# Kernel tuning notes

Hardware: AMD Instinct MI355X
Metric: run time of the kernel (lower is better)

The kernel has to match this reference:

```python
import jax, jax.numpy as jnp
import numpy as np

TREE = 128
BASIC = 128
EPS = 1e-5


def layer_norm(x, g, b):
    m = jnp.mean(x, axis=-1, keepdims=True)
    v = jnp.mean((x - m) ** 2, axis=-1, keepdims=True)
    return (x - m) * jax.lax.rsqrt(v + EPS) * g + b


def setup_inputs() -> dict:
    key = jax.random.key(0)
    ks = jax.random.split(key, 32)
    n2, n1, n0 = 320000, 80000, 20000
    inp = {
        'subtree_h_top': jax.random.normal(ks[0], (n2, TREE), jnp.float32),
        'atom_x_1': jax.random.normal(ks[1], (n1, BASIC), jnp.float32),
        'atom_x_0': jax.random.normal(ks[2], (n0, BASIC), jnp.float32),
        'bond_x_2': jax.random.normal(ks[3], (n2, BASIC), jnp.float32),
        'bond_x_1': jax.random.normal(ks[4], (n1, BASIC), jnp.float32),
        'branch_W1': jax.random.normal(ks[5], (2, TREE + BASIC, TREE), jnp.float32) * 0.05,
        'branch_b1': jnp.zeros((2, TREE), jnp.float32),
        'branch_g1': jnp.ones((2, TREE), jnp.float32),
        'branch_beta1': jnp.zeros((2, TREE), jnp.float32),
        'branch_W2': jax.random.normal(ks[6], (2, TREE, TREE), jnp.float32) * 0.05,
        'branch_b2': jnp.zeros((2, TREE), jnp.float32),
        'branch_g2': jnp.ones((2, TREE), jnp.float32),
        'branch_beta2': jnp.zeros((2, TREE), jnp.float32),
        'sub_W1': jax.random.normal(ks[7], (2, BASIC + TREE, TREE), jnp.float32) * 0.05,
        'sub_b1': jnp.zeros((2, TREE), jnp.float32),
        'sub_g1': jnp.ones((2, TREE), jnp.float32),
        'sub_beta1': jnp.zeros((2, TREE), jnp.float32),
        'sub_W2': jax.random.normal(ks[8], (2, TREE, TREE), jnp.float32) * 0.05,
        'sub_b2': jnp.zeros((2, TREE), jnp.float32),
        'sub_g2': jnp.ones((2, TREE), jnp.float32),
        'sub_beta2': jnp.zeros((2, TREE), jnp.float32),
        'head_W': jax.random.normal(ks[9], (2, BASIC + TREE, TREE), jnp.float32) * 0.05,
        'head_b': jnp.zeros((2, TREE), jnp.float32),
        'head_g': jnp.ones((2, TREE), jnp.float32),
        'head_beta': jnp.zeros((2, TREE), jnp.float32),
        'src_2': jax.random.randint(ks[10], (n2,), 0, n2),
        'dst_2': jax.random.randint(ks[11], (n2,), 0, n1),
        'src_1': jax.random.randint(ks[12], (n1,), 0, n1),
        'dst_1': jax.random.randint(ks[13], (n1,), 0, n0),
    }
    return inp


def reference(subtree_h_top, atom_x_1, atom_x_0, bond_x_2, bond_x_1,
              branch_W1, branch_b1, branch_g1, branch_beta1,
              branch_W2, branch_b2, branch_g2, branch_beta2,
              sub_W1, sub_b1, sub_g1, sub_beta1,
              sub_W2, sub_b2, sub_g2, sub_beta2,
              head_W, head_b, head_g, head_beta,
              src_2, dst_2, src_1, dst_1):
    relu = jax.nn.relu
    h = subtree_h_top  # subtree_h of level tree_level nodes
    atom_xs = (atom_x_1, atom_x_0)
    bond_xs = (bond_x_2, bond_x_1)
    srcs = (src_2, src_1)
    dsts = (dst_2, dst_1)
    for i in range(2):  # i=0 -> k=2, i=1 -> k=1 (fixed small loop over tree levels)
        ax = atom_xs[i]
        # Branch_Update: edge MLP on [subtree_h[src], bond_x]
        ex = jnp.concatenate([h[srcs[i]], bond_xs[i]], axis=-1)  # [E, tree+basic]
        bh = relu(layer_norm(ex @ branch_W1[i] + branch_b1[i], branch_g1[i], branch_beta1[i]))
        bh = relu(layer_norm(bh @ branch_W2[i] + branch_b2[i], branch_g2[i], branch_beta2[i]))
        # fn.sum aggregation per destination (head) node
        agg = jax.ops.segment_sum(bh, dsts[i], num_segments=ax.shape[0])
        # Tree_Update_Sep
        sx = jnp.concatenate([ax, agg], axis=-1)  # [N, basic+tree]
        f = relu(layer_norm(sx @ sub_W1[i] + sub_b1[i], sub_g1[i], sub_beta1[i]))
        f = relu(layer_norm(f @ sub_W2[i] + sub_b2[i], sub_g2[i], sub_beta2[i]))
        th = jnp.concatenate([ax, f], axis=-1)
        h = relu(layer_norm(th @ head_W[i] + head_b[i], head_g[i], head_beta[i]))
    return h  # subtree_h of atom_0 nodes: [n0, tree_dim]
```

## Files before the change

### kernel.cpp

```cpp
#include <hip/hip_runtime.h>


#define D   128
#define TE  64
#define XS  264

typedef float  f32x4 __attribute__((ext_vector_type(4)));
typedef _Float16 f16x8 __attribute__((ext_vector_type(8)));

__device__ __forceinline__ unsigned short f2h(float f) {
    union { _Float16 h; unsigned short u; } x;
    x.h = (_Float16)f;
    return x.u;
}

__global__ __launch_bounds__(256) void pack_w(
    const float* __restrict__ brW1, const float* __restrict__ brW2,
    const float* __restrict__ sW1,  const float* __restrict__ sW2,
    const float* __restrict__ hW,   unsigned short* __restrict__ Wp)
{
    int p = blockIdx.x * 256 + threadIdx.x;
    const float* src; int off, K;
    if (p < 65536)       { src = brW1; off = 0;      K = 256; }
    else if (p < 98304)  { src = brW2; off = 65536;  K = 128; }
    else if (p < 163840) { src = sW1;  off = 98304;  K = 256; }
    else if (p < 196608) { src = sW2;  off = 163840; K = 128; }
    else                 { src = hW;   off = 196608; K = 256; }
    int q = p - off, lvl, r;
    if (K == 256) { lvl = q >> 15; r = q & 32767; }
    else          { lvl = q >> 14; r = q & 16383; }
    int kb = r >> 12, n = (r >> 5) & 127, kk = r & 31;
    Wp[p] = f2h(src[(size_t)lvl * K * 128 + (size_t)(kb * 32 + kk) * 128 + n]);
}


__global__ __launch_bounds__(256) void csr_hist(
    const int* __restrict__ dA, int EA, const int* __restrict__ dB, int EB,
    int* __restrict__ cnt, int AOFFv)
{
    int i = blockIdx.x * 256 + threadIdx.x;
    if (i < EA)               atomicAdd(cnt + dA[i], 1);
    else if (i - EA < EB)     atomicAdd(cnt + AOFFv + dB[i - EA], 1);
}

__global__ __launch_bounds__(256) void csr_scanA(
    const int* __restrict__ cnt, int* __restrict__ inc, int* __restrict__ bsum,
    int nbA, int AOFFv)
{
    __shared__ int lds[256];
    int b = blockIdx.x, t = threadIdx.x;
    int lb, ebase, bs;
    if (b < nbA) { lb = b;       ebase = 0;     bs = lb; }
    else         { lb = b - nbA; ebase = AOFFv; bs = 128 + lb; }
    int idx = ebase + lb * 1024 + t * 4;
    int s0 = cnt[idx], s1 = cnt[idx + 1], s2 = cnt[idx + 2], s3 = cnt[idx + 3];
    int p1 = s0 + s1, p2 = p1 + s2, p3 = p2 + s3;
    lds[t] = p3; __syncthreads();
#pragma unroll
    for (int o = 1; o < 256; o <<= 1) {
        int v = (t >= o) ? lds[t - o] : 0;
        __syncthreads();
        lds[t] += v;
        __syncthreads();
    }
    int ex = lds[t] - p3;
    inc[idx] = ex + s0; inc[idx + 1] = ex + p1; inc[idx + 2] = ex + p2; inc[idx + 3] = ex + p3;
    if (t == 255) bsum[bs] = lds[255];
}

__global__ __launch_bounds__(256) void csr_scanB(int* __restrict__ bsum, int nbA, int nbB)
{
    __shared__ int lds[256];
    int t = threadIdx.x, seg = t >> 7, i = t & 127;
    int n = seg ? nbB : nbA;
    lds[t] = (i < n) ? bsum[t] : 0;
    __syncthreads();
#pragma unroll
    for (int o = 1; o < 128; o <<= 1) {
        int v = (i >= o) ? lds[t - o] : 0;
        __syncthreads();
        lds[t] += v;
        __syncthreads();
    }
    if (i < n) bsum[t] = lds[t];
}

__global__ __launch_bounds__(256) void csr_scanC(
    const int* __restrict__ cnt, int* __restrict__ inc, const int* __restrict__ bsum,
    int* __restrict__ cursor, int nbA, int AOFFv)
{
    int b = blockIdx.x, t = threadIdx.x;
    int lb, ebase, bs;
    if (b < nbA) { lb = b;       ebase = 0;     bs = lb; }
    else         { lb = b - nbA; ebase = AOFFv; bs = 128 + lb; }
    int carry = (lb > 0) ? bsum[bs - 1] : 0;
    int idx = ebase + lb * 1024 + t * 4;
#pragma unroll
    for (int j = 0; j < 4; ++j) {
        int v = inc[idx + j] + carry;
        inc[idx + j] = v;
        cursor[idx + j] = v - cnt[idx + j];
    }
}

__global__ __launch_bounds__(256) void csr_pos(
    const int* __restrict__ dA, int EA, const int* __restrict__ dB, int EB,
    int* __restrict__ cursor, int* __restrict__ posA, int* __restrict__ posB, int AOFFv)
{
    int i = blockIdx.x * 256 + threadIdx.x;
    if (i < EA)           posA[i] = atomicAdd(cursor + dA[i], 1);
    else if (i - EA < EB) posB[i - EA] = atomicAdd(cursor + AOFFv + dB[i - EA], 1);
}


template<int KB>
__device__ __forceinline__ void gemm_f16(const unsigned short* s_in, int stride,
    const unsigned short* __restrict__ Wp, int rb, int cb, int n15, int q, f32x4 acc[2][4])
{
    f32x4 zero = {0.f, 0.f, 0.f, 0.f};
#pragma unroll
    for (int m = 0; m < 2; ++m)
#pragma unroll
        for (int ct = 0; ct < 4; ++ct) acc[m][ct] = zero;
#pragma unroll
    for (int kb = 0; kb < KB; ++kb) {
        f16x8 af0 = *(const f16x8*)(s_in + (rb + n15) * stride + kb * 32 + q * 8);
        f16x8 af1 = *(const f16x8*)(s_in + (rb + 16 + n15) * stride + kb * 32 + q * 8);
        const unsigned short* wb = Wp + (size_t)kb * 4096 + q * 8;
#pragma unroll
        for (int ct = 0; ct < 4; ++ct) {
            f16x8 bf = *(const f16x8*)(wb + (cb + ct * 16 + n15) * 32);
            acc[0][ct] = __builtin_amdgcn_mfma_f32_16x16x32_f16(af0, bf, acc[0][ct], 0, 0, 0);
            acc[1][ct] = __builtin_amdgcn_mfma_f32_16x16x32_f16(af1, bf, acc[1][ct], 0, 0, 0);
        }
    }
}

__device__ __forceinline__ void ln_relu(f32x4 acc[2][4],
    const float* __restrict__ b, const float* __restrict__ g, const float* __restrict__ be,
    float* s_red, float* s_ms, int rb, int cb, int n15, int q, int wcol, int t)
{
#pragma unroll
    for (int ct = 0; ct < 4; ++ct) {
        float bb = b[cb + ct * 16 + n15];
#pragma unroll
        for (int m = 0; m < 2; ++m)
#pragma unroll
            for (int r = 0; r < 4; ++r) acc[m][ct][r] += bb;
    }
    float sum[2][4], ss[2][4];
#pragma unroll
    for (int m = 0; m < 2; ++m)
#pragma unroll
        for (int r = 0; r < 4; ++r) {
            sum[m][r] = acc[m][0][r] + acc[m][1][r] + acc[m][2][r] + acc[m][3][r];
            ss[m][r]  = acc[m][0][r]*acc[m][0][r] + acc[m][1][r]*acc[m][1][r]
                      + acc[m][2][r]*acc[m][2][r] + acc[m][3][r]*acc[m][3][r];
        }
#pragma unroll
    for (int off = 1; off < 16; off <<= 1) {
#pragma unroll
        for (int m = 0; m < 2; ++m)
#pragma unroll
            for (int r = 0; r < 4; ++r) {
                sum[m][r] += __shfl_xor(sum[m][r], off, 64);
                ss[m][r]  += __shfl_xor(ss[m][r],  off, 64);
            }
    }
    if (n15 == 0) {
#pragma unroll
        for (int m = 0; m < 2; ++m)
#pragma unroll
            for (int r = 0; r < 4; ++r) {
                int row = rb + m * 16 + q * 4 + r;
                s_red[row * 4 + wcol * 2 + 0] = sum[m][r];
                s_red[row * 4 + wcol * 2 + 1] = ss[m][r];
            }
    }
    __syncthreads();
    if (t < TE) {
        float sm = s_red[t * 4 + 0] + s_red[t * 4 + 2];
        float sq = s_red[t * 4 + 1] + s_red[t * 4 + 3];
        float mean = sm * (1.f / 128.f);
        float var  = sq * (1.f / 128.f) - mean * mean;
        s_ms[t * 2 + 0] = mean;
        s_ms[t * 2 + 1] = rsqrtf(var + 1e-5f);
    }
    __syncthreads();
#pragma unroll
    for (int ct = 0; ct < 4; ++ct) {
        float gg = g[cb + ct * 16 + n15], bb = be[cb + ct * 16 + n15];
#pragma unroll
        for (int m = 0; m < 2; ++m)
#pragma unroll
            for (int r = 0; r < 4; ++r) {
                int row = rb + m * 16 + q * 4 + r;
                float v = (acc[m][ct][r] - s_ms[row * 2 + 0]) * s_ms[row * 2 + 1] * gg + bb;
                acc[m][ct][r] = fmaxf(v, 0.f);
            }
    }
}

template<bool HBF16, bool CSR>
__global__ __launch_bounds__(256, 4) void edge_mlp(
    const void* __restrict__ hsrc, const float* __restrict__ bond,
    const int* __restrict__ src, const int* __restrict__ dstpos,
    const unsigned short* __restrict__ Wp1, const unsigned short* __restrict__ Wp2,
    const float* __restrict__ b1, const float* __restrict__ g1, const float* __restrict__ be1,
    const float* __restrict__ b2, const float* __restrict__ g2, const float* __restrict__ be2,
    float* __restrict__ agg, unsigned short* __restrict__ ebh, int E)
{
    __shared__ unsigned short s_x[TE * XS];
    __shared__ float s_red[TE * 4];
    __shared__ float s_ms[TE * 2];
    __shared__ int s_src[TE], s_idx[TE];
    unsigned short* s_y = s_x + 128;

    int t = threadIdx.x, eb = blockIdx.x * TE;
    if (t < TE) {
        int ge = eb + t;
        s_src[t] = (ge < E) ? src[ge] : -1;
        s_idx[t] = (ge < E) ? dstpos[ge] : -1;
    }
    __syncthreads();

    if (HBF16) {
        const unsigned short* hp = (const unsigned short*)hsrc;
        for (int c = t; c < TE * 16; c += 256) {
            int row = c >> 4, k8 = c & 15;
            int s = s_src[row];
            uint4 v = make_uint4(0, 0, 0, 0);
            if (s >= 0) v = *(const uint4*)(hp + (size_t)s * 128 + k8 * 8);
            *(uint4*)(s_x + row * XS + k8 * 8) = v;
        }
    } else {
        const float* hp = (const float*)hsrc;
        for (int c = t; c < TE * 32; c += 256) {
            int row = c >> 5, k4 = c & 31;
            int s = s_src[row];
            float4 v = make_float4(0, 0, 0, 0);
            if (s >= 0) v = *(const float4*)(hp + (size_t)s * 128 + k4 * 4);
            ushort4 o; o.x = f2h(v.x); o.y = f2h(v.y); o.z = f2h(v.z); o.w = f2h(v.w);
            *(ushort4*)(s_x + row * XS + k4 * 4) = o;
        }
    }
    for (int c = t; c < TE * 32; c += 256) {
        int row = c >> 5, k4 = c & 31;
        int ge = eb + row;
        float4 v = make_float4(0, 0, 0, 0);
        if (ge < E) v = *(const float4*)(bond + (size_t)ge * 128 + k4 * 4);
        ushort4 o; o.x = f2h(v.x); o.y = f2h(v.y); o.z = f2h(v.z); o.w = f2h(v.w);
        *(ushort4*)(s_x + row * XS + 128 + k4 * 4) = o;
    }
    __syncthreads();

    int l = t & 63, w = t >> 6;
    int n15 = l & 15, q = l >> 4;
    int rb = (w & 1) * 32, cb = (w >> 1) * 64, wcol = w >> 1;

    f32x4 acc[2][4];
    gemm_f16<8>(s_x, XS, Wp1, rb, cb, n15, q, acc);
    ln_relu(acc, b1, g1, be1, s_red, s_ms, rb, cb, n15, q, wcol, t);
#pragma unroll
    for (int m = 0; m < 2; ++m)
#pragma unroll
        for (int ct = 0; ct < 4; ++ct)
#pragma unroll
            for (int r = 0; r < 4; ++r)
                s_y[(rb + m * 16 + q * 4 + r) * XS + cb + ct * 16 + n15] = f2h(acc[m][ct][r]);
    __syncthreads();
    gemm_f16<4>(s_y, XS, Wp2, rb, cb, n15, q, acc);
    ln_relu(acc, b2, g2, be2, s_red, s_ms, rb, cb, n15, q, wcol, t);

    if (CSR) {
#pragma unroll
        for (int m = 0; m < 2; ++m)
#pragma unroll
            for (int ct = 0; ct < 4; ++ct)
#pragma unroll
                for (int r = 0; r < 4; ++r)
                    s_x[(rb + m * 16 + q * 4 + r) * XS + cb + ct * 16 + n15] = f2h(acc[m][ct][r]);
        __syncthreads();
        for (int c = t; c < TE * 16; c += 256) {
            int row = c >> 4, k8 = c & 15;
            int p = s_idx[row];
            if (p >= 0)
                *(uint4*)(ebh + (size_t)p * 128 + k8 * 8) =
                    *(const uint4*)(s_x + row * XS + k8 * 8);
        }
    } else {
#pragma unroll
        for (int m = 0; m < 2; ++m)
#pragma unroll
            for (int ct = 0; ct < 4; ++ct)
#pragma unroll
                for (int r = 0; r < 4; ++r) {
                    int row = rb + m * 16 + q * 4 + r;
                    int gd = s_idx[row];
                    if (gd >= 0)
                        atomicAdd(agg + (size_t)gd * D + cb + ct * 16 + n15, acc[m][ct][r]);
                }
    }
}

template<bool OUT_F16, bool CSR>
__global__ __launch_bounds__(256, 4) void node_mlp(
    const float* __restrict__ ax, const float* __restrict__ agg,
    const int* __restrict__ inc, const unsigned short* __restrict__ ebh,
    const unsigned short* __restrict__ Wp1, const unsigned short* __restrict__ Wp2,
    const unsigned short* __restrict__ Wp3,
    const float* __restrict__ b1, const float* __restrict__ g1, const float* __restrict__ be1,
    const float* __restrict__ b2, const float* __restrict__ g2, const float* __restrict__ be2,
    const float* __restrict__ b3, const float* __restrict__ g3, const float* __restrict__ be3,
    void* __restrict__ out, int N)
{
    __shared__ unsigned short s_x[TE * XS];
    __shared__ float s_red[TE * 4];
    __shared__ float s_ms[TE * 2];
    __shared__ int s_beg[TE], s_end[TE];
    unsigned short* s_y = s_x + 128;

    int t = threadIdx.x, nb = blockIdx.x * TE;

    if (CSR && t < TE) {
        int gr = nb + t, b0 = 0, e0 = 0;
        if (gr < N) { e0 = inc[gr]; b0 = (gr == 0) ? 0 : inc[gr - 1]; }
        s_beg[t] = b0; s_end[t] = e0;
    }

    for (int c = t; c < TE * 32; c += 256) {
        int row = c >> 5, k4 = c & 31;
        int gr = nb + row;
        float4 v = make_float4(0, 0, 0, 0);
        if (gr < N) v = *(const float4*)(ax + (size_t)gr * 128 + k4 * 4);
        ushort4 o; o.x = f2h(v.x); o.y = f2h(v.y); o.z = f2h(v.z); o.w = f2h(v.w);
        *(ushort4*)(s_x + row * XS + k4 * 4) = o;
    }

    if (CSR) {
        __syncthreads();
        int r = t >> 2, s4 = t & 3;
        float a[32];
#pragma unroll
        for (int k = 0; k < 32; ++k) a[k] = 0.f;
        int jb = s_beg[r], je = s_end[r];
        for (int j = jb; j < je; ++j) {
            const unsigned short* rp = ebh + (size_t)j * 128 + s4 * 32;
            f16x8 v0 = *(const f16x8*)rp;
            f16x8 v1 = *(const f16x8*)(rp + 8);
            f16x8 v2 = *(const f16x8*)(rp + 16);
            f16x8 v3 = *(const f16x8*)(rp + 24);
#pragma unroll
            for (int k = 0; k < 8; ++k) {
                a[k]      += (float)v0[k];
                a[8 + k]  += (float)v1[k];
                a[16 + k] += (float)v2[k];
                a[24 + k] += (float)v3[k];
            }
        }
        unsigned short* op = s_x + r * XS + 128 + s4 * 32;
#pragma unroll
        for (int blk = 0; blk < 4; ++blk) {
            f16x8 h;
#pragma unroll
            for (int k = 0; k < 8; ++k) h[k] = (_Float16)a[blk * 8 + k];
            *(f16x8*)(op + blk * 8) = h;
        }
    } else {
        for (int c = t; c < TE * 32; c += 256) {
            int row = c >> 5, k4 = c & 31;
            int gr = nb + row;
            float4 v = make_float4(0, 0, 0, 0);
            if (gr < N) v = *(const float4*)(agg + (size_t)gr * 128 + k4 * 4);
            ushort4 o; o.x = f2h(v.x); o.y = f2h(v.y); o.z = f2h(v.z); o.w = f2h(v.w);
            *(ushort4*)(s_x + row * XS + 128 + k4 * 4) = o;
        }
    }
    __syncthreads();

    int l = t & 63, w = t >> 6;
    int n15 = l & 15, q = l >> 4;
    int rb = (w & 1) * 32, cb = (w >> 1) * 64, wcol = w >> 1;

    f32x4 acc[2][4];
    gemm_f16<8>(s_x, XS, Wp1, rb, cb, n15, q, acc);
    ln_relu(acc, b1, g1, be1, s_red, s_ms, rb, cb, n15, q, wcol, t);
#pragma unroll
    for (int m = 0; m < 2; ++m)
#pragma unroll
        for (int ct = 0; ct < 4; ++ct)
#pragma unroll
            for (int r = 0; r < 4; ++r)
                s_y[(rb + m * 16 + q * 4 + r) * XS + cb + ct * 16 + n15] = f2h(acc[m][ct][r]);
    __syncthreads();
    gemm_f16<4>(s_y, XS, Wp2, rb, cb, n15, q, acc);
    ln_relu(acc, b2, g2, be2, s_red, s_ms, rb, cb, n15, q, wcol, t);
#pragma unroll
    for (int m = 0; m < 2; ++m)
#pragma unroll
        for (int ct = 0; ct < 4; ++ct)
#pragma unroll
            for (int r = 0; r < 4; ++r)
                s_x[(rb + m * 16 + q * 4 + r) * XS + 128 + cb + ct * 16 + n15] = f2h(acc[m][ct][r]);
    __syncthreads();
    gemm_f16<8>(s_x, XS, Wp3, rb, cb, n15, q, acc);
    ln_relu(acc, b3, g3, be3, s_red, s_ms, rb, cb, n15, q, wcol, t);

#pragma unroll
    for (int m = 0; m < 2; ++m)
#pragma unroll
        for (int ct = 0; ct < 4; ++ct)
#pragma unroll
            for (int r = 0; r < 4; ++r) {
                int row = rb + m * 16 + q * 4 + r;
                int gr = nb + row;
                int col = cb + ct * 16 + n15;
                if (gr < N) {
                    if (OUT_F16)
                        ((unsigned short*)out)[(size_t)gr * D + col] = f2h(acc[m][ct][r]);
                    else
                        ((float*)out)[(size_t)gr * D + col] = acc[m][ct][r];
                }
            }
}

extern "C" void kernel_launch(void* const* d_in, const int* in_sizes, int n_in,
                              void* d_out, int out_size, void* d_ws, size_t ws_size,
                              hipStream_t stream)
{
    const float* h2   = (const float*)d_in[0];
    const float* ax1  = (const float*)d_in[1];
    const float* ax0  = (const float*)d_in[2];
    const float* bx2  = (const float*)d_in[3];
    const float* bx1  = (const float*)d_in[4];
    const float* brW1 = (const float*)d_in[5];
    const float* brb1 = (const float*)d_in[6];
    const float* brg1 = (const float*)d_in[7];
    const float* brbe1= (const float*)d_in[8];
    const float* brW2 = (const float*)d_in[9];
    const float* brb2 = (const float*)d_in[10];
    const float* brg2 = (const float*)d_in[11];
    const float* brbe2= (const float*)d_in[12];
    const float* sW1  = (const float*)d_in[13];
    const float* sb1  = (const float*)d_in[14];
    const float* sg1  = (const float*)d_in[15];
    const float* sbe1 = (const float*)d_in[16];
    const float* sW2  = (const float*)d_in[17];
    const float* sb2  = (const float*)d_in[18];
    const float* sg2  = (const float*)d_in[19];
    const float* sbe2 = (const float*)d_in[20];
    const float* hW   = (const float*)d_in[21];
    const float* hb   = (const float*)d_in[22];
    const float* hg   = (const float*)d_in[23];
    const float* hbe  = (const float*)d_in[24];
    const int*   src2 = (const int*)d_in[25];
    const int*   dst2 = (const int*)d_in[26];
    const int*   src1 = (const int*)d_in[27];
    const int*   dst1 = (const int*)d_in[28];

    int n2 = in_sizes[0] / D;
    int n1 = in_sizes[1] / D;
    int n0 = in_sizes[2] / D;

    unsigned short* Wp = (unsigned short*)d_ws;

    const unsigned short* pBr1[2] = { Wp + 0,      Wp + 32768 };
    const unsigned short* pBr2[2] = { Wp + 65536,  Wp + 65536  + 16384 };
    const unsigned short* pS1 [2] = { Wp + 98304,  Wp + 98304  + 32768 };
    const unsigned short* pS2 [2] = { Wp + 163840, Wp + 163840 + 16384 };
    const unsigned short* pH  [2] = { Wp + 196608, Wp + 196608 + 32768 };

    int nbA = (n1 + 1023) / 1024, nbB = (n0 + 1023) / 1024;
    int AOFFv = nbA * 1024;
    size_t AN = (size_t)AOFFv + (size_t)nbB * 1024;
    auto al = [](size_t x) { return (x + 255) & ~(size_t)255; };
    size_t o = 524288;
    size_t cnt_o  = o; o = al(o + AN * 4);
    size_t inc_o  = o; o = al(o + AN * 4);
    size_t cur_o  = o; o = al(o + AN * 4);
    size_t bsum_o = o; o = al(o + 1024);
    size_t posA_o = o; o = al(o + (size_t)n2 * 4);
    size_t posB_o = o; o = al(o + (size_t)n1 * 4);
    size_t h1_o   = o; o = al(o + (size_t)n1 * 256);
    size_t ebh_o  = o; o = al(o + (size_t)n2 * 256);
    bool use_csr = (ws_size >= o) && (nbA <= 128) && (nbB <= 128);

    pack_w<<<dim3(1024), dim3(256), 0, stream>>>(brW1, brW2, sW1, sW2, hW, Wp);

    if (use_csr) {
        int*            cnt    = (int*)((char*)d_ws + cnt_o);
        int*            inc    = (int*)((char*)d_ws + inc_o);
        int*            cursor = (int*)((char*)d_ws + cur_o);
        int*            bsum   = (int*)((char*)d_ws + bsum_o);
        int*            posA   = (int*)((char*)d_ws + posA_o);
        int*            posB   = (int*)((char*)d_ws + posB_o);
        unsigned short* h1     = (unsigned short*)((char*)d_ws + h1_o);
        unsigned short* ebh    = (unsigned short*)((char*)d_ws + ebh_o);

        int EG = (n2 + n1 + 255) / 256;
        hipMemsetAsync(cnt, 0, AN * 4, stream);
        csr_hist <<<dim3(EG),        dim3(256), 0, stream>>>(dst2, n2, dst1, n1, cnt, AOFFv);
        csr_scanA<<<dim3(nbA + nbB), dim3(256), 0, stream>>>(cnt, inc, bsum, nbA, AOFFv);
        csr_scanB<<<dim3(1),         dim3(256), 0, stream>>>(bsum, nbA, nbB);
        csr_scanC<<<dim3(nbA + nbB), dim3(256), 0, stream>>>(cnt, inc, bsum, cursor, nbA, AOFFv);
        csr_pos  <<<dim3(EG),        dim3(256), 0, stream>>>(dst2, n2, dst1, n1, cursor, posA, posB, AOFFv);

        edge_mlp<false, true><<<dim3((n2 + TE - 1) / TE), dim3(256), 0, stream>>>(
            h2, bx2, src2, posA, pBr1[0], pBr2[0],
            brb1, brg1, brbe1, brb2, brg2, brbe2, nullptr, ebh, n2);
        node_mlp<true, true><<<dim3((n1 + TE - 1) / TE), dim3(256), 0, stream>>>(
            ax1, nullptr, inc, ebh, pS1[0], pS2[0], pH[0],
            sb1, sg1, sbe1, sb2, sg2, sbe2, hb, hg, hbe, h1, n1);

        edge_mlp<true, true><<<dim3((n1 + TE - 1) / TE), dim3(256), 0, stream>>>(
            h1, bx1, src1, posB, pBr1[1], pBr2[1],
            brb1 + D, brg1 + D, brbe1 + D, brb2 + D, brg2 + D, brbe2 + D, nullptr, ebh, n1);
        node_mlp<false, true><<<dim3((n0 + TE - 1) / TE), dim3(256), 0, stream>>>(
            ax0, nullptr, inc + AOFFv, ebh, pS1[1], pS2[1], pH[1],
            sb1 + D, sg1 + D, sbe1 + D, sb2 + D, sg2 + D, sbe2 + D,
            hb + D, hg + D, hbe + D, d_out, n0);
    } else {
        float*          agg = (float*)((char*)d_ws + 524288);
        unsigned short* h1  = (unsigned short*)(agg + (size_t)n1 * D);

        hipMemsetAsync(agg, 0, (size_t)n1 * D * sizeof(float), stream);
        edge_mlp<false, false><<<dim3((n2 + TE - 1) / TE), dim3(256), 0, stream>>>(
            h2, bx2, src2, dst2, pBr1[0], pBr2[0],
            brb1, brg1, brbe1, brb2, brg2, brbe2, agg, nullptr, n2);
        node_mlp<true, false><<<dim3((n1 + TE - 1) / TE), dim3(256), 0, stream>>>(
            ax1, agg, nullptr, nullptr, pS1[0], pS2[0], pH[0],
            sb1, sg1, sbe1, sb2, sg2, sbe2, hb, hg, hbe, h1, n1);

        hipMemsetAsync(agg, 0, (size_t)n0 * D * sizeof(float), stream);
        edge_mlp<true, false><<<dim3((n1 + TE - 1) / TE), dim3(256), 0, stream>>>(
            h1, bx1, src1, dst1, pBr1[1], pBr2[1],
            brb1 + D, brg1 + D, brbe1 + D, brb2 + D, brg2 + D, brbe2 + D, agg, nullptr, n1);
        node_mlp<false, false><<<dim3((n0 + TE - 1) / TE), dim3(256), 0, stream>>>(
            ax0, agg, nullptr, nullptr, pS1[1], pS2[1], pH[1],
            sb1 + D, sg1 + D, sbe1 + D, sb2 + D, sg2 + D, sbe2 + D,
            hb + D, hg + D, hbe + D, d_out, n0);
    }
}
```

Before: 682.6 us.

## Add persistent prefetching edge MLP and pre-convert subtree features to fp16

Adds a persistent-block edge MLP kernel that loads the next tile's gathered h rows, bond rows and destination positions into registers while the current tile's two GEMM+LayerNorm stages run. This hides gather latency behind compute. A separate conversion kernel first turns the top-level subtree_h into fp16, so the random gather reads half the bytes. node_mlp becomes grid-strided with a capped grid. The new path needs extra workspace, and the kernel drops occupancy to 3 blocks per SM because of the added prefetch registers.

```diff
diff --git a/kernel.cpp b/kernel.cpp
--- a/kernel.cpp
+++ b/kernel.cpp
@@ -33,6 +33,22 @@
     Wp[p] = f2h(src[(size_t)lvl * K * 128 + (size_t)(kb * 32 + kk) * 128 + n]);
 }
 
+__global__ __launch_bounds__(256) void conv_h(
+    const float* __restrict__ in, unsigned short* __restrict__ out, long n)
+{
+    long i = (long)blockIdx.x * 256 + threadIdx.x;
+    long stride = (long)gridDim.x * 256;
+    for (; i < n; i += stride) {
+        float4 a = ((const float4*)in)[i * 2];
+        float4 b = ((const float4*)in)[i * 2 + 1];
+        ushort4 o1, o2;
+        o1.x = f2h(a.x); o1.y = f2h(a.y); o1.z = f2h(a.z); o1.w = f2h(a.w);
+        o2.x = f2h(b.x); o2.y = f2h(b.y); o2.z = f2h(b.z); o2.w = f2h(b.w);
+        ((ushort4*)out)[i * 2]     = o1;
+        ((ushort4*)out)[i * 2 + 1] = o2;
+    }
+}
+
 
 __global__ __launch_bounds__(256) void csr_hist(
     const int* __restrict__ dA, int EA, const int* __restrict__ dB, int EB,
@@ -201,6 +217,124 @@
     }
 }
 
+__global__ __launch_bounds__(256, 3) void edge_mlp_pf(
+    const unsigned short* __restrict__ hsrc, const float* __restrict__ bond,
+    const int* __restrict__ src, const int* __restrict__ dstpos,
+    const unsigned short* __restrict__ Wp1, const unsigned short* __restrict__ Wp2,
+    const float* __restrict__ b1, const float* __restrict__ g1, const float* __restrict__ be1,
+    const float* __restrict__ b2, const float* __restrict__ g2, const float* __restrict__ be2,
+    unsigned short* __restrict__ ebh, int E, int ntiles)
+{
+    __shared__ unsigned short s_x[TE * XS];
+    __shared__ float s_red[TE * 4];
+    __shared__ float s_ms[TE * 2];
+    unsigned short* s_y = s_x + 128;
+
+    int t = threadIdx.x;
+    int l = t & 63, w = t >> 6;
+    int n15 = l & 15, q = l >> 4;
+    int rb = (w & 1) * 32, cb = (w >> 1) * 64, wcol = w >> 1;
+    int hrow = t >> 4, k8 = t & 15;
+    int brow = t >> 5, k4 = t & 31;
+
+    int tile0 = blockIdx.x;
+    if (tile0 >= ntiles) return;
+
+    int cidx[4];
+    {
+        int eb = tile0 * TE;
+#pragma unroll
+        for (int j = 0; j < 4; ++j) {
+            int ge = eb + hrow + 16 * j;
+            int sv = (ge < E) ? src[ge] : -1;
+            cidx[j] = (ge < E) ? dstpos[ge] : -1;
+            uint4 v = make_uint4(0, 0, 0, 0);
+            if (sv >= 0) v = *(const uint4*)(hsrc + (size_t)sv * 128 + k8 * 8);
+            *(uint4*)(s_x + (hrow + 16 * j) * XS + k8 * 8) = v;
+        }
+#pragma unroll
+        for (int i = 0; i < 8; ++i) {
+            int ge = eb + brow + 8 * i;
+            float4 v = make_float4(0, 0, 0, 0);
+            if (ge < E) v = *(const float4*)(bond + (size_t)ge * 128 + k4 * 4);
+            ushort4 o; o.x = f2h(v.x); o.y = f2h(v.y); o.z = f2h(v.z); o.w = f2h(v.w);
+            *(ushort4*)(s_x + (brow + 8 * i) * XS + 128 + k4 * 4) = o;
+        }
+    }
+
+    for (int tile = tile0; tile < ntiles; tile += gridDim.x) {
+        __syncthreads();
+
+        int ntile = tile + gridDim.x;
+        bool has_next = (ntile < ntiles);
+        uint4  ph[4];
+        float4 pb[8];
+        int    nidx[4];
+        if (has_next) {
+            int eb = ntile * TE;
+#pragma unroll
+            for (int j = 0; j < 4; ++j) {
+                int ge = eb + hrow + 16 * j;
+                int sv = (ge < E) ? src[ge] : -1;
+                nidx[j] = (ge < E) ? dstpos[ge] : -1;
+                ph[j] = make_uint4(0, 0, 0, 0);
+                if (sv >= 0) ph[j] = *(const uint4*)(hsrc + (size_t)sv * 128 + k8 * 8);
+            }
+#pragma unroll
+            for (int i = 0; i < 8; ++i) {
+                int ge = eb + brow + 8 * i;
+                pb[i] = make_float4(0, 0, 0, 0);
+                if (ge < E) pb[i] = *(const float4*)(bond + (size_t)ge * 128 + k4 * 4);
+            }
+            __builtin_amdgcn_sched_barrier(0);
+        }
+
+        f32x4 acc[2][4];
+        gemm_f16<8>(s_x, XS, Wp1, rb, cb, n15, q, acc);
+        ln_relu(acc, b1, g1, be1, s_red, s_ms, rb, cb, n15, q, wcol, t);
+#pragma unroll
+        for (int m = 0; m < 2; ++m)
+#pragma unroll
+            for (int ct = 0; ct < 4; ++ct)
+#pragma unroll
+                for (int r = 0; r < 4; ++r)
+                    s_y[(rb + m * 16 + q * 4 + r) * XS + cb + ct * 16 + n15] = f2h(acc[m][ct][r]);
+        __syncthreads();
+        gemm_f16<4>(s_y, XS, Wp2, rb, cb, n15, q, acc);
+        ln_relu(acc, b2, g2, be2, s_red, s_ms, rb, cb, n15, q, wcol, t);
+
+#pragma unroll
+        for (int m = 0; m < 2; ++m)
+#pragma unroll
+            for (int ct = 0; ct < 4; ++ct)
+#pragma unroll
+                for (int r = 0; r < 4; ++r)
+                    s_x[(rb + m * 16 + q * 4 + r) * XS + cb + ct * 16 + n15] = f2h(acc[m][ct][r]);
+        __syncthreads();
+#pragma unroll
+        for (int j = 0; j < 4; ++j) {
+            if (cidx[j] >= 0)
+                *(uint4*)(ebh + (size_t)cidx[j] * 128 + k8 * 8) =
+                    *(const uint4*)(s_x + (hrow + 16 * j) * XS + k8 * 8);
+        }
+        __syncthreads();
+
+        if (has_next) {
+#pragma unroll
+            for (int j = 0; j < 4; ++j)
+                *(uint4*)(s_x + (hrow + 16 * j) * XS + k8 * 8) = ph[j];
+#pragma unroll
+            for (int i = 0; i < 8; ++i) {
+                ushort4 o;
+                o.x = f2h(pb[i].x); o.y = f2h(pb[i].y); o.z = f2h(pb[i].z); o.w = f2h(pb[i].w);
+                *(ushort4*)(s_x + (brow + 8 * i) * XS + 128 + k4 * 4) = o;
+            }
+#pragma unroll
+            for (int j = 0; j < 4; ++j) cidx[j] = nidx[j];
+        }
+    }
+}
+
 template<bool HBF16, bool CSR>
 __global__ __launch_bounds__(256, 4) void edge_mlp(
     const void* __restrict__ hsrc, const float* __restrict__ bond,
@@ -312,7 +446,7 @@
     const float* __restrict__ b1, const float* __restrict__ g1, const float* __restrict__ be1,
     const float* __restrict__ b2, const float* __restrict__ g2, const float* __restrict__ be2,
     const float* __restrict__ b3, const float* __restrict__ g3, const float* __restrict__ be3,
-    void* __restrict__ out, int N)
+    void* __restrict__ out, int N, int ntiles)
 {
     __shared__ unsigned short s_x[TE * XS];
     __shared__ float s_red[TE * 4];
@@ -320,108 +454,110 @@
     __shared__ int s_beg[TE], s_end[TE];
     unsigned short* s_y = s_x + 128;
 
-    int t = threadIdx.x, nb = blockIdx.x * TE;
-
-    if (CSR && t < TE) {
-        int gr = nb + t, b0 = 0, e0 = 0;
-        if (gr < N) { e0 = inc[gr]; b0 = (gr == 0) ? 0 : inc[gr - 1]; }
-        s_beg[t] = b0; s_end[t] = e0;
-    }
-
-    for (int c = t; c < TE * 32; c += 256) {
-        int row = c >> 5, k4 = c & 31;
-        int gr = nb + row;
-        float4 v = make_float4(0, 0, 0, 0);
-        if (gr < N) v = *(const float4*)(ax + (size_t)gr * 128 + k4 * 4);
-        ushort4 o; o.x = f2h(v.x); o.y = f2h(v.y); o.z = f2h(v.z); o.w = f2h(v.w);
-        *(ushort4*)(s_x + row * XS + k4 * 4) = o;
-    }
-
-    if (CSR) {
-        __syncthreads();
-        int r = t >> 2, s4 = t & 3;
-        float a[32];
-#pragma unroll
-        for (int k = 0; k < 32; ++k) a[k] = 0.f;
-        int jb = s_beg[r], je = s_end[r];
-        for (int j = jb; j < je; ++j) {
-            const unsigned short* rp = ebh + (size_t)j * 128 + s4 * 32;
-            f16x8 v0 = *(const f16x8*)rp;
-            f16x8 v1 = *(const f16x8*)(rp + 8);
-            f16x8 v2 = *(const f16x8*)(rp + 16);
-            f16x8 v3 = *(const f16x8*)(rp + 24);
-#pragma unroll
-            for (int k = 0; k < 8; ++k) {
-                a[k]      += (float)v0[k];
-                a[8 + k]  += (float)v1[k];
-                a[16 + k] += (float)v2[k];
-                a[24 + k] += (float)v3[k];
-            }
-        }
-        unsigned short* op = s_x + r * XS + 128 + s4 * 32;
-#pragma unroll
-        for (int blk = 0; blk < 4; ++blk) {
-            f16x8 h;
-#pragma unroll
-            for (int k = 0; k < 8; ++k) h[k] = (_Float16)a[blk * 8 + k];
-            *(f16x8*)(op + blk * 8) = h;
-        }
-    } else {
+    int t = threadIdx.x;
+    int l = t & 63, w = t >> 6;
+    int n15 = l & 15, q = l >> 4;
+    int rb = (w & 1) * 32, cb = (w >> 1) * 64, wcol = w >> 1;
+
+    for (int tile = blockIdx.x; tile < ntiles; tile += gridDim.x) {
+        int nb = tile * TE;
+        if (CSR && t < TE) {
+            int gr = nb + t, b0 = 0, e0 = 0;
+            if (gr < N) { e0 = inc[gr]; b0 = (gr == 0) ? 0 : inc[gr - 1]; }
+            s_beg[t] = b0; s_end[t] = e0;
+        }
+
         for (int c = t; c < TE * 32; c += 256) {
             int row = c >> 5, k4 = c & 31;
             int gr = nb + row;
             float4 v = make_float4(0, 0, 0, 0);
-            if (gr < N) v = *(const float4*)(agg + (size_t)gr * 128 + k4 * 4);
+            if (gr < N) v = *(const float4*)(ax + (size_t)gr * 128 + k4 * 4);
             ushort4 o; o.x = f2h(v.x); o.y = f2h(v.y); o.z = f2h(v.z); o.w = f2h(v.w);
-            *(ushort4*)(s_x + row * XS + 128 + k4 * 4) = o;
-        }
-    }
-    __syncthreads();
-
-    int l = t & 63, w = t >> 6;
-    int n15 = l & 15, q = l >> 4;
-    int rb = (w & 1) * 32, cb = (w >> 1) * 64, wcol = w >> 1;
-
-    f32x4 acc[2][4];
-    gemm_f16<8>(s_x, XS, Wp1, rb, cb, n15, q, acc);
-    ln_relu(acc, b1, g1, be1, s_red, s_ms, rb, cb, n15, q, wcol, t);
-#pragma unroll
-    for (int m = 0; m < 2; ++m)
-#pragma unroll
-        for (int ct = 0; ct < 4; ++ct)
-#pragma unroll
-            for (int r = 0; r < 4; ++r)
-                s_y[(rb + m * 16 + q * 4 + r) * XS + cb + ct * 16 + n15] = f2h(acc[m][ct][r]);
-    __syncthreads();
-    gemm_f16<4>(s_y, XS, Wp2, rb, cb, n15, q, acc);
-    ln_relu(acc, b2, g2, be2, s_red, s_ms, rb, cb, n15, q, wcol, t);
-#pragma unroll
-    for (int m = 0; m < 2; ++m)
-#pragma unroll
-        for (int ct = 0; ct < 4; ++ct)
-#pragma unroll
-            for (int r = 0; r < 4; ++r)
-                s_x[(rb + m * 16 + q * 4 + r) * XS + 128 + cb + ct * 16 + n15] = f2h(acc[m][ct][r]);
-    __syncthreads();
-    gemm_f16<8>(s_x, XS, Wp3, rb, cb, n15, q, acc);
-    ln_relu(acc, b3, g3, be3, s_red, s_ms, rb, cb, n15, q, wcol, t);
-
-#pragma unroll
-    for (int m = 0; m < 2; ++m)
-#pragma unroll
-        for (int ct = 0; ct < 4; ++ct)
-#pragma unroll
-            for (int r = 0; r < 4; ++r) {
-                int row = rb + m * 16 + q * 4 + r;
+            *(ushort4*)(s_x + row * XS + k4 * 4) = o;
+        }
+
+        if (CSR) {
+            __syncthreads();
+            int r = t >> 2, s4 = t & 3;
+            float a[32];
+#pragma unroll
+            for (int k = 0; k < 32; ++k) a[k] = 0.f;
+            int jb = s_beg[r], je = s_end[r];
+            for (int j = jb; j < je; ++j) {
+                const unsigned short* rp = ebh + (size_t)j * 128 + s4 * 32;
+                f16x8 v0 = *(const f16x8*)rp;
+                f16x8 v1 = *(const f16x8*)(rp + 8);
+                f16x8 v2 = *(const f16x8*)(rp + 16);
+                f16x8 v3 = *(const f16x8*)(rp + 24);
+#pragma unroll
+                for (int k = 0; k < 8; ++k) {
+                    a[k]      += (float)v0[k];
+                    a[8 + k]  += (float)v1[k];
+                    a[16 + k] += (float)v2[k];
+                    a[24 + k] += (float)v3[k];
+                }
+            }
+            unsigned short* op = s_x + r * XS + 128 + s4 * 32;
+#pragma unroll
+            for (int blk = 0; blk < 4; ++blk) {
+                f16x8 h;
+#pragma unroll
+                for (int k = 0; k < 8; ++k) h[k] = (_Float16)a[blk * 8 + k];
+                *(f16x8*)(op + blk * 8) = h;
+            }
+        } else {
+            for (int c = t; c < TE * 32; c += 256) {
+                int row = c >> 5, k4 = c & 31;
                 int gr = nb + row;
-                int col = cb + ct * 16 + n15;
-                if (gr < N) {
-                    if (OUT_F16)
-                        ((unsigned short*)out)[(size_t)gr * D + col] = f2h(acc[m][ct][r]);
-                    else
-                        ((float*)out)[(size_t)gr * D + col] = acc[m][ct][r];
+                float4 v = make_float4(0, 0, 0, 0);
+                if (gr < N) v = *(const float4*)(agg + (size_t)gr * 128 + k4 * 4);
+                ushort4 o; o.x = f2h(v.x); o.y = f2h(v.y); o.z = f2h(v.z); o.w = f2h(v.w);
+                *(ushort4*)(s_x + row * XS + 128 + k4 * 4) = o;
+            }
+        }
+        __syncthreads();
+
+        f32x4 acc[2][4];
+        gemm_f16<8>(s_x, XS, Wp1, rb, cb, n15, q, acc);
+        ln_relu(acc, b1, g1, be1, s_red, s_ms, rb, cb, n15, q, wcol, t);
+#pragma unroll
+        for (int m = 0; m < 2; ++m)
+#pragma unroll
+            for (int ct = 0; ct < 4; ++ct)
+#pragma unroll
+                for (int r = 0; r < 4; ++r)
+                    s_y[(rb + m * 16 + q * 4 + r) * XS + cb + ct * 16 + n15] = f2h(acc[m][ct][r]);
+        __syncthreads();
+        gemm_f16<4>(s_y, XS, Wp2, rb, cb, n15, q, acc);
+        ln_relu(acc, b2, g2, be2, s_red, s_ms, rb, cb, n15, q, wcol, t);
+#pragma unroll
+        for (int m = 0; m < 2; ++m)
+#pragma unroll
+            for (int ct = 0; ct < 4; ++ct)
+#pragma unroll
+                for (int r = 0; r < 4; ++r)
+                    s_x[(rb + m * 16 + q * 4 + r) * XS + 128 + cb + ct * 16 + n15] = f2h(acc[m][ct][r]);
+        __syncthreads();
+        gemm_f16<8>(s_x, XS, Wp3, rb, cb, n15, q, acc);
+        ln_relu(acc, b3, g3, be3, s_red, s_ms, rb, cb, n15, q, wcol, t);
+
+#pragma unroll
+        for (int m = 0; m < 2; ++m)
+#pragma unroll
+            for (int ct = 0; ct < 4; ++ct)
+#pragma unroll
+                for (int r = 0; r < 4; ++r) {
+                    int row = rb + m * 16 + q * 4 + r;
+                    int gr = nb + row;
+                    int col = cb + ct * 16 + n15;
+                    if (gr < N) {
+                        if (OUT_F16)
+                            ((unsigned short*)out)[(size_t)gr * D + col] = f2h(acc[m][ct][r]);
+                        else
+                            ((float*)out)[(size_t)gr * D + col] = acc[m][ct][r];
+                    }
                 }
-            }
+    }
 }
 
 extern "C" void kernel_launch(void* const* d_in, const int* in_sizes, int n_in,
@@ -483,11 +619,19 @@
     size_t posB_o = o; o = al(o + (size_t)n1 * 4);
     size_t h1_o   = o; o = al(o + (size_t)n1 * 256);
     size_t ebh_o  = o; o = al(o + (size_t)n2 * 256);
-    bool use_csr = (ws_size >= o) && (nbA <= 128) && (nbB <= 128);
+    size_t o_csr  = o;
+    size_t h2h_o  = o; o = al(o + (size_t)n2 * 256);
+    size_t o_full = o;
+    bool csr_ok = (nbA <= 128) && (nbB <= 128);
+    bool tier1 = csr_ok && (ws_size >= o_full);
+    bool tier2 = !tier1 && csr_ok && (ws_size >= o_csr);
 
     pack_w<<<dim3(1024), dim3(256), 0, stream>>>(brW1, brW2, sW1, sW2, hW, Wp);
 
-    if (use_csr) {
+    int t2e = (n2 + TE - 1) / TE, t1e = (n1 + TE - 1) / TE;
+    int t1n = (n1 + TE - 1) / TE, t0n = (n0 + TE - 1) / TE;
+
+    if (tier1 || tier2) {
         int*            cnt    = (int*)((char*)d_ws + cnt_o);
         int*            inc    = (int*)((char*)d_ws + inc_o);
         int*            cursor = (int*)((char*)d_ws + cur_o);
@@ -496,6 +640,7 @@
         int*            posB   = (int*)((char*)d_ws + posB_o);
         unsigned short* h1     = (unsigned short*)((char*)d_ws + h1_o);
         unsigned short* ebh    = (unsigned short*)((char*)d_ws + ebh_o);
+        unsigned short* h2h    = (unsigned short*)((char*)d_ws + h2h_o);
 
         int EG = (n2 + n1 + 255) / 256;
         hipMemsetAsync(cnt, 0, AN * 4, stream);
@@ -505,39 +650,57 @@
         csr_scanC<<<dim3(nbA + nbB), dim3(256), 0, stream>>>(cnt, inc, bsum, cursor, nbA, AOFFv);
         csr_pos  <<<dim3(EG),        dim3(256), 0, stream>>>(dst2, n2, dst1, n1, cursor, posA, posB, AOFFv);
 
-        edge_mlp<false, true><<<dim3((n2 + TE - 1) / TE), dim3(256), 0, stream>>>(
-            h2, bx2, src2, posA, pBr1[0], pBr2[0],
-            brb1, brg1, brbe1, brb2, brg2, brbe2, nullptr, ebh, n2);
-        node_mlp<true, true><<<dim3((n1 + TE - 1) / TE), dim3(256), 0, stream>>>(
-            ax1, nullptr, inc, ebh, pS1[0], pS2[0], pH[0],
-            sb1, sg1, sbe1, sb2, sg2, sbe2, hb, hg, hbe, h1, n1);
-
-        edge_mlp<true, true><<<dim3((n1 + TE - 1) / TE), dim3(256), 0, stream>>>(
-            h1, bx1, src1, posB, pBr1[1], pBr2[1],
-            brb1 + D, brg1 + D, brbe1 + D, brb2 + D, brg2 + D, brbe2 + D, nullptr, ebh, n1);
-        node_mlp<false, true><<<dim3((n0 + TE - 1) / TE), dim3(256), 0, stream>>>(
-            ax0, nullptr, inc + AOFFv, ebh, pS1[1], pS2[1], pH[1],
-            sb1 + D, sg1 + D, sbe1 + D, sb2 + D, sg2 + D, sbe2 + D,
-            hb + D, hg + D, hbe + D, d_out, n0);
+        if (tier1) {
+            conv_h<<<dim3(2048), dim3(256), 0, stream>>>(h2, h2h, (long)n2 * 16);
+
+            edge_mlp_pf<<<dim3(min(t2e, 768)), dim3(256), 0, stream>>>(
+                h2h, bx2, src2, posA, pBr1[0], pBr2[0],
+                brb1, brg1, brbe1, brb2, brg2, brbe2, ebh, n2, t2e);
+            node_mlp<true, true><<<dim3(min(t1n, 1024)), dim3(256), 0, stream>>>(
+                ax1, nullptr, inc, ebh, pS1[0], pS2[0], pH[0],
+                sb1, sg1, sbe1, sb2, sg2, sbe2, hb, hg, hbe, h1, n1, t1n);
+
+            edge_mlp_pf<<<dim3(min(t1e, 768)), dim3(256), 0, stream>>>(
+                h1, bx1, src1, posB, pBr1[1], pBr2[1],
+                brb1 + D, brg1 + D, brbe1 + D, brb2 + D, brg2 + D, brbe2 + D, ebh, n1, t1e);
+            node_mlp<false, true><<<dim3(min(t0n, 1024)), dim3(256), 0, stream>>>(
+                ax0, nullptr, inc + AOFFv, ebh, pS1[1], pS2[1], pH[1],
+                sb1 + D, sg1 + D, sbe1 + D, sb2 + D, sg2 + D, sbe2 + D,
+                hb + D, hg + D, hbe + D, d_out, n0, t0n);
+        } else {
+            edge_mlp<false, true><<<dim3(t2e), dim3(256), 0, stream>>>(
+                h2, bx2, src2, posA, pBr1[0], pBr2[0],
+                brb1, brg1, brbe1, brb2, brg2, brbe2, nullptr, ebh, n2);
+            node_mlp<true, true><<<dim3(min(t1n, 1024)), dim3(256), 0, stream>>>(
+                ax1, nullptr, inc, ebh, pS1[0], pS2[0], pH[0],
+                sb1, sg1, sbe1, sb2, sg2, sbe2, hb, hg, hbe, h1, n1, t1n);
+            edge_mlp<true, true><<<dim3(t1e), dim3(256), 0, stream>>>(
+                h1, bx1, src1, posB, pBr1[1], pBr2[1],
+                brb1 + D, brg1 + D, brbe1 + D, brb2 + D, brg2 + D, brbe2 + D, nullptr, ebh, n1);
+            node_mlp<false, true><<<dim3(min(t0n, 1024)), dim3(256), 0, stream>>>(
+                ax0, nullptr, inc + AOFFv, ebh, pS1[1], pS2[1], pH[1],
+                sb1 + D, sg1 + D, sbe1 + D, sb2 + D, sg2 + D, sbe2 + D,
+                hb + D, hg + D, hbe + D, d_out, n0, t0n);
+        }
     } else {
         float*          agg = (float*)((char*)d_ws + 524288);
         unsigned short* h1  = (unsigned short*)(agg + (size_t)n1 * D);
 
         hipMemsetAsync(agg, 0, (size_t)n1 * D * sizeof(float), stream);
-        edge_mlp<false, false><<<dim3((n2 + TE - 1) / TE), dim3(256), 0, stream>>>(
+        edge_mlp<false, false><<<dim3(t2e), dim3(256), 0, stream>>>(
             h2, bx2, src2, dst2, pBr1[0], pBr2[0],
             brb1, brg1, brbe1, brb2, brg2, brbe2, agg, nullptr, n2);
-        node_mlp<true, false><<<dim3((n1 + TE - 1) / TE), dim3(256), 0, stream>>>(
+        node_mlp<true, false><<<dim3(min(t1n, 1024)), dim3(256), 0, stream>>>(
             ax1, agg, nullptr, nullptr, pS1[0], pS2[0], pH[0],
-            sb1, sg1, sbe1, sb2, sg2, sbe2, hb, hg, hbe, h1, n1);
+            sb1, sg1, sbe1, sb2, sg2, sbe2, hb, hg, hbe, h1, n1, t1n);
 
         hipMemsetAsync(agg, 0, (size_t)n0 * D * sizeof(float), stream);
-        edge_mlp<true, false><<<dim3((n1 + TE - 1) / TE), dim3(256), 0, stream>>>(
+        edge_mlp<true, false><<<dim3(t1e), dim3(256), 0, stream>>>(
             h1, bx1, src1, dst1, pBr1[1], pBr2[1],
             brb1 + D, brg1 + D, brbe1 + D, brb2 + D, brg2 + D, brbe2 + D, agg, nullptr, n1);
-        node_mlp<false, false><<<dim3((n0 + TE - 1) / TE), dim3(256), 0, stream>>>(
+        node_mlp<false, false><<<dim3(min(t0n, 1024)), dim3(256), 0, stream>>>(
             ax0, agg, nullptr, nullptr, pS1[1], pS2[1], pH[1],
             sb1 + D, sg1 + D, sbe1 + D, sb2 + D, sg2 + D, sbe2 + D,
-            hb + D, hg + D, hbe + D, d_out, n0);
-    }
-}
+            hb + D, hg + D, hbe + D, d_out, n0, t0n);
+    }
+}
```

After: 1.330 ms. 1.95x slower.

## Fuse weight packing and CSR construction into one cooperative grid-synced kernel

Applied to the files above, without the earlier changes.

Replaces the memset, pack_w and five CSR build kernels (hist, three scan phases, position assignment) with one cooperative kernel of 256 blocks that separates the phases with grid.sync(). The goal is to remove the launch overhead and idle gaps between several small kernels that run ahead of the edge and node MLPs. If the cooperative launch fails, the code falls back to the original multi-kernel sequence. Grid syncs cost time of their own, and the scan is spread over only 256 blocks, so a phase could become slower than its standalone kernel.

```diff
diff --git a/kernel.cpp b/kernel.cpp
--- a/kernel.cpp
+++ b/kernel.cpp
@@ -1,4 +1,7 @@
 #include <hip/hip_runtime.h>
+#include <hip/hip_cooperative_groups.h>
+
+namespace cg = cooperative_groups;
 
 
 #define D   128
@@ -14,12 +17,11 @@
     return x.u;
 }
 
-__global__ __launch_bounds__(256) void pack_w(
+__device__ __forceinline__ void pack_one(int p,
     const float* __restrict__ brW1, const float* __restrict__ brW2,
     const float* __restrict__ sW1,  const float* __restrict__ sW2,
     const float* __restrict__ hW,   unsigned short* __restrict__ Wp)
 {
-    int p = blockIdx.x * 256 + threadIdx.x;
     const float* src; int off, K;
     if (p < 65536)       { src = brW1; off = 0;      K = 256; }
     else if (p < 98304)  { src = brW2; off = 65536;  K = 128; }
@@ -31,6 +33,96 @@
     else          { lvl = q >> 14; r = q & 16383; }
     int kb = r >> 12, n = (r >> 5) & 127, kk = r & 31;
     Wp[p] = f2h(src[(size_t)lvl * K * 128 + (size_t)(kb * 32 + kk) * 128 + n]);
+}
+
+__global__ __launch_bounds__(256) void pack_w(
+    const float* __restrict__ brW1, const float* __restrict__ brW2,
+    const float* __restrict__ sW1,  const float* __restrict__ sW2,
+    const float* __restrict__ hW,   unsigned short* __restrict__ Wp)
+{
+    pack_one(blockIdx.x * 256 + threadIdx.x, brW1, brW2, sW1, sW2, hW, Wp);
+}
+
+__global__ __launch_bounds__(256, 2) void csr_coop(
+    const float* __restrict__ brW1, const float* __restrict__ brW2,
+    const float* __restrict__ sW1,  const float* __restrict__ sW2,
+    const float* __restrict__ hW,   unsigned short* __restrict__ Wp,
+    const int* __restrict__ dA, int EA, const int* __restrict__ dB, int EB,
+    int* __restrict__ cnt, int* __restrict__ inc, int* __restrict__ cursor,
+    int* __restrict__ bsum, int* __restrict__ posA, int* __restrict__ posB,
+    int AOFFv, int nbA, int nbB, int AN)
+{
+    cg::grid_group grid = cg::this_grid();
+    __shared__ int lds[256];
+    int t = threadIdx.x, b = blockIdx.x;
+    int gtid = b * 256 + t, gsz = gridDim.x * 256;
+
+    for (int i = gtid; i < AN; i += gsz) cnt[i] = 0;
+    for (int p = gtid; p < 262144; p += gsz)
+        pack_one(p, brW1, brW2, sW1, sW2, hW, Wp);
+    grid.sync();
+
+    for (int i = gtid; i < EA + EB; i += gsz) {
+        if (i < EA) atomicAdd(cnt + dA[i], 1);
+        else        atomicAdd(cnt + AOFFv + dB[i - EA], 1);
+    }
+    grid.sync();
+
+    bool actA = (b < nbA), actB = (b >= 128 && b < 128 + nbB);
+    int lb = actA ? b : b - 128;
+    int ebase = actA ? 0 : AOFFv;
+    int bs = actA ? lb : 128 + lb;
+    if (actA || actB) {
+        int idx = ebase + lb * 1024 + t * 4;
+        int s0 = cnt[idx], s1 = cnt[idx + 1], s2 = cnt[idx + 2], s3 = cnt[idx + 3];
+        int p1 = s0 + s1, p2 = p1 + s2, p3 = p2 + s3;
+        lds[t] = p3; __syncthreads();
+#pragma unroll
+        for (int o = 1; o < 256; o <<= 1) {
+            int v = (t >= o) ? lds[t - o] : 0;
+            __syncthreads();
+            lds[t] += v;
+            __syncthreads();
+        }
+        int ex = lds[t] - p3;
+        inc[idx] = ex + s0; inc[idx + 1] = ex + p1;
+        inc[idx + 2] = ex + p2; inc[idx + 3] = ex + p3;
+        if (t == 255) bsum[bs] = lds[255];
+    }
+    grid.sync();
+
+    if (b == 0) {
+        int seg = t >> 7, i = t & 127;
+        int n = seg ? nbB : nbA;
+        lds[t] = (i < n) ? bsum[t] : 0;
+        __syncthreads();
+#pragma unroll
+        for (int o = 1; o < 128; o <<= 1) {
+            int v = (i >= o) ? lds[t - o] : 0;
+            __syncthreads();
+            lds[t] += v;
+            __syncthreads();
+        }
+        if (i < n) bsum[t] = lds[t];
+    }
+    grid.sync();
+
+    if (actA || actB) {
+        int carry = (lb > 0) ? bsum[bs - 1] : 0;
+        int idx = ebase + lb * 1024 + t * 4;
+#pragma unroll
+        for (int j = 0; j < 4; ++j) {
+            int v = inc[idx + j] + carry;
+            inc[idx + j] = v;
+            cursor[idx + j] = v - cnt[idx + j];
+        }
+    }
+    grid.sync();
+
+    for (int i = gtid; i < EA + EB; i += gsz) {
+        if (i < EA) posA[i] = atomicAdd(cursor + dA[i], 1);
+        else        posB[i - EA] = atomicAdd(cursor + AOFFv + dB[i - EA], 1);
+    }
 }
 
 
@@ -472,20 +564,22 @@
 
     int nbA = (n1 + 1023) / 1024, nbB = (n0 + 1023) / 1024;
     int AOFFv = nbA * 1024;
-    size_t AN = (size_t)AOFFv + (size_t)nbB * 1024;
+    int AN = AOFFv + nbB * 1024;
     auto al = [](size_t x) { return (x + 255) & ~(size_t)255; };
     size_t o = 524288;
-    size_t cnt_o  = o; o = al(o + AN * 4);
-    size_t inc_o  = o; o = al(o + AN * 4);
-    size_t cur_o  = o; o = al(o + AN * 4);
+    size_t cnt_o  = o; o = al(o + (size_t)AN * 4);
+    size_t inc_o  = o; o = al(o + (size_t)AN * 4);
+    size_t cur_o  = o; o = al(o + (size_t)AN * 4);
     size_t bsum_o = o; o = al(o + 1024);
     size_t posA_o = o; o = al(o + (size_t)n2 * 4);
     size_t posB_o = o; o = al(o + (size_t)n1 * 4);
     size_t h1_o   = o; o = al(o + (size_t)n1 * 256);
     size_t ebh_o  = o; o = al(o + (size_t)n2 * 256);
-    bool use_csr = (ws_size >= o) && (nbA <= 128) && (nbB <= 128);
-
-    pack_w<<<dim3(1024), dim3(256), 0, stream>>>(brW1, brW2, sW1, sW2, hW, Wp);
+    size_t o_csr  = o;
+    bool use_csr = (nbA <= 128) && (nbB <= 128) && (ws_size >= o_csr);
+
+    int t2e = (n2 + TE - 1) / TE, t1e = (n1 + TE - 1) / TE;
+    int t1n = (n1 + TE - 1) / TE, t0n = (n0 + TE - 1) / TE;
 
     if (use_csr) {
         int*            cnt    = (int*)((char*)d_ws + cnt_o);
@@ -497,25 +591,42 @@
         unsigned short* h1     = (unsigned short*)((char*)d_ws + h1_o);
         unsigned short* ebh    = (unsigned short*)((char*)d_ws + ebh_o);
 
-        int EG = (n2 + n1 + 255) / 256;
-        hipMemsetAsync(cnt, 0, AN * 4, stream);
-        csr_hist <<<dim3(EG),        dim3(256), 0, stream>>>(dst2, n2, dst1, n1, cnt, AOFFv);
-        csr_scanA<<<dim3(nbA + nbB), dim3(256), 0, stream>>>(cnt, inc, bsum, nbA, AOFFv);
-        csr_scanB<<<dim3(1),         dim3(256), 0, stream>>>(bsum, nbA, nbB);
-        csr_scanC<<<dim3(nbA + nbB), dim3(256), 0, stream>>>(cnt, inc, bsum, cursor, nbA, AOFFv);
-        csr_pos  <<<dim3(EG),        dim3(256), 0, stream>>>(dst2, n2, dst1, n1, cursor, posA, posB, AOFFv);
-
-        edge_mlp<false, true><<<dim3((n2 + TE - 1) / TE), dim3(256), 0, stream>>>(
+        {
+            const float *a0 = brW1, *a1 = brW2, *a2 = sW1, *a3 = sW2, *a4 = hW;
+            unsigned short* a5 = Wp;
+            const int* a6 = dst2; int a7 = n2;
+            const int* a8 = dst1; int a9 = n1;
+            int *a10 = cnt, *a11 = inc, *a12 = cursor, *a13 = bsum;
+            int *a14 = posA, *a15 = posB;
+            int a16 = AOFFv, a17 = nbA, a18 = nbB, a19 = AN;
+            void* args[] = { &a0, &a1, &a2, &a3, &a4, &a5, &a6, &a7, &a8, &a9,
+                             &a10, &a11, &a12, &a13, &a14, &a15, &a16, &a17, &a18, &a19 };
+            hipError_t cerr = hipLaunchCooperativeKernel(
+                (const void*)csr_coop, dim3(256), dim3(256), args, 0, stream);
+            if (cerr != hipSuccess) {
+                (void)hipGetLastError();
+                pack_w<<<dim3(1024), dim3(256), 0, stream>>>(brW1, brW2, sW1, sW2, hW, Wp);
+                int EG = (n2 + n1 + 255) / 256;
+                hipMemsetAsync(cnt, 0, (size_t)AN * 4, stream);
+                csr_hist <<<dim3(EG),        dim3(256), 0, stream>>>(dst2, n2, dst1, n1, cnt, AOFFv);
+                csr_scanA<<<dim3(nbA + nbB), dim3(256), 0, stream>>>(cnt, inc, bsum, nbA, AOFFv);
+                csr_scanB<<<dim3(1),         dim3(256), 0, stream>>>(bsum, nbA, nbB);
+                csr_scanC<<<dim3(nbA + nbB), dim3(256), 0, stream>>>(cnt, inc, bsum, cursor, nbA, AOFFv);
+                csr_pos  <<<dim3(EG),        dim3(256), 0, stream>>>(dst2, n2, dst1, n1, cursor, posA, posB, AOFFv);
+            }
+        }
+
+        edge_mlp<false, true><<<dim3(t2e), dim3(256), 0, stream>>>(
             h2, bx2, src2, posA, pBr1[0], pBr2[0],
             brb1, brg1, brbe1, brb2, brg2, brbe2, nullptr, ebh, n2);
-        node_mlp<true, true><<<dim3((n1 + TE - 1) / TE), dim3(256), 0, stream>>>(
+        node_mlp<true, true><<<dim3(t1n), dim3(256), 0, stream>>>(
             ax1, nullptr, inc, ebh, pS1[0], pS2[0], pH[0],
             sb1, sg1, sbe1, sb2, sg2, sbe2, hb, hg, hbe, h1, n1);
 
-        edge_mlp<true, true><<<dim3((n1 + TE - 1) / TE), dim3(256), 0, stream>>>(
+        edge_mlp<true, true><<<dim3(t1e), dim3(256), 0, stream>>>(
             h1, bx1, src1, posB, pBr1[1], pBr2[1],
             brb1 + D, brg1 + D, brbe1 + D, brb2 + D, brg2 + D, brbe2 + D, nullptr, ebh, n1);
-        node_mlp<false, true><<<dim3((n0 + TE - 1) / TE), dim3(256), 0, stream>>>(
+        node_mlp<false, true><<<dim3(t0n), dim3(256), 0, stream>>>(
             ax0, nullptr, inc + AOFFv, ebh, pS1[1], pS2[1], pH[1],
             sb1 + D, sg1 + D, sbe1 + D, sb2 + D, sg2 + D, sbe2 + D,
             hb + D, hg + D, hbe + D, d_out, n0);
@@ -523,19 +634,21 @@
         float*          agg = (float*)((char*)d_ws + 524288);
         unsigned short* h1  = (unsigned short*)(agg + (size_t)n1 * D);
 
+        pack_w<<<dim3(1024), dim3(256), 0, stream>>>(brW1, brW2, sW1, sW2, hW, Wp);
+
         hipMemsetAsync(agg, 0, (size_t)n1 * D * sizeof(float), stream);
-        edge_mlp<false, false><<<dim3((n2 + TE - 1) / TE), dim3(256), 0, stream>>>(
+        edge_mlp<false, false><<<dim3(t2e), dim3(256), 0, stream>>>(
             h2, bx2, src2, dst2, pBr1[0], pBr2[0],
             brb1, brg1, brbe1, brb2, brg2, brbe2, agg, nullptr, n2);
-        node_mlp<true, false><<<dim3((n1 + TE - 1) / TE), dim3(256), 0, stream>>>(
+        node_mlp<true, false><<<dim3(t1n), dim3(256), 0, stream>>>(
             ax1, agg, nullptr, nullptr, pS1[0], pS2[0], pH[0],
             sb1, sg1, sbe1, sb2, sg2, sbe2, hb, hg, hbe, h1, n1);
 
         hipMemsetAsync(agg, 0, (size_t)n0 * D * sizeof(float), stream);
-        edge_mlp<true, false><<<dim3((n1 + TE - 1) / TE), dim3(256), 0, stream>>>(
+        edge_mlp<true, false><<<dim3(t1e), dim3(256), 0, stream>>>(
             h1, bx1, src1, dst1, pBr1[1], pBr2[1],
             brb1 + D, brg1 + D, brbe1 + D, brb2 + D, brg2 + D, brbe2 + D, agg, nullptr, n1);
-        node_mlp<false, false><<<dim3((n0 + TE - 1) / TE), dim3(256), 0, stream>>>(
+        node_mlp<false, false><<<dim3(t0n), dim3(256), 0, stream>>>(
             ax0, agg, nullptr, nullptr, pS1[1], pS2[1], pH[1],
             sb1 + D, sg1 + D, sbe1 + D, sb2 + D, sg2 + D, sbe2 + D,
             hb + D, hg + D, hbe + D, d_out, n0);
```

Result: slower. 854.2 us (+25.1%).
